# Optimization experiments

Hardware: AMD Instinct MI355X
Metric: run time of the kernel (lower is better)

Reference implementation:

```python
import jax, jax.numpy as jnp
import numpy as np

WEIGHT = 0.1  # init weight

# 6-connectivity (scipy generate_binary_structure(3,1)) neighbor reductions

def _nmin(x, fill):
    p = jnp.pad(x, 1, constant_values=fill)
    return jnp.minimum(
        jnp.minimum(jnp.minimum(p[:-2, 1:-1, 1:-1], p[2:, 1:-1, 1:-1]),
                    jnp.minimum(p[1:-1, :-2, 1:-1], p[1:-1, 2:, 1:-1])),
        jnp.minimum(p[1:-1, 1:-1, :-2], p[1:-1, 1:-1, 2:]))


def _nor(x):
    p = jnp.pad(x, 1, constant_values=False)
    return (p[:-2, 1:-1, 1:-1] | p[2:, 1:-1, 1:-1] |
            p[1:-1, :-2, 1:-1] | p[1:-1, 2:, 1:-1] |
            p[1:-1, 1:-1, :-2] | p[1:-1, 1:-1, 2:])


def _nand(x):
    # border_value=0 in scipy.binary_erosion -> pad with False
    p = jnp.pad(x, 1, constant_values=False)
    return (p[:-2, 1:-1, 1:-1] & p[2:, 1:-1, 1:-1] &
            p[1:-1, :-2, 1:-1] & p[1:-1, 2:, 1:-1] &
            p[1:-1, 1:-1, :-2] & p[1:-1, 1:-1, 2:])


def _cc_count(mask):
    # connected-component count via min-label propagation (6-connectivity),
    # equivalent to scipy.ndimage.label(...)[1]
    n = mask.size
    idx = jnp.arange(n, dtype=jnp.int32).reshape(mask.shape)
    big = jnp.int32(n)
    lbl0 = jnp.where(mask, idx, big)

    def body(c):
        lbl, _ = c
        new = jnp.where(mask, jnp.minimum(lbl, _nmin(lbl, big)), big)
        return new, jnp.any(new != lbl)

    lbl, _ = jax.lax.while_loop(lambda c: c[1], body, (lbl0, jnp.bool_(True)))
    # roots: voxels whose label equals their own index
    return jnp.sum(mask & (lbl == idx)).astype(jnp.int32)


def _cavity_volume(mask):
    # binary_fill_holes: background not reachable from the border
    bg = ~mask
    border = jnp.ones(mask.shape, bool).at[1:-1, 1:-1, 1:-1].set(False)
    r0 = bg & border

    def body(c):
        r, _ = c
        new = bg & (r | _nor(r))
        return new, jnp.any(new != r)

    reach, _ = jax.lax.while_loop(lambda c: c[1], body, (r0, jnp.bool_(True)))
    return jnp.sum(bg & ~reach).astype(jnp.int32)


def _betti(mask):
    b0 = _cc_count(mask)
    eroded = mask & _nand(mask)  # binary_erosion, iterations=1
    b0e = _cc_count(eroded)
    b1 = jnp.maximum(jnp.int32(0), b0 - b0e)
    b2 = _cavity_volume(mask) // 100
    return jnp.stack([b0, b1, b2]).astype(jnp.float32)


def setup_inputs() -> dict:
    key = jax.random.key(0)
    k1, k2 = jax.random.split(key)
    B, C, D, H, W = 2, 4, 64, 128, 128
    pred = jax.random.normal(k1, (B, C, D, H, W), dtype=jnp.float32)
    target = jax.random.randint(k2, (B, D, H, W), 0, C, dtype=jnp.int32)
    return {"pred": pred, "target": target}


def reference(pred, target):
    B, C = pred.shape[0], pred.shape[1]
    vol = pred.shape[2:]
    prob = jax.nn.softmax(pred, axis=1)
    # foreground classes 1..C-1, flattened to [B*(C-1), D, H, W]
    pred_masks = (prob[:, 1:] > 0.5).reshape((-1,) + vol)
    cls = jnp.arange(1, C, dtype=target.dtype).reshape(1, C - 1, 1, 1, 1)
    tgt_masks = (target[:, None] == cls).reshape((-1,) + vol)
    pb = jax.vmap(_betti)(pred_masks)  # [B*(C-1), 3]
    tb = jax.vmap(_betti)(tgt_masks)
    count = B * (C - 1)
    return WEIGHT * jnp.abs(pb - tb).sum() / count
```

## Files before the change

### kernel.cpp

```cpp
#include <hip/hip_runtime.h>
#include <stdint.h>

#define DD 64
#define HH 128
#define WW 128
#define NVOX (DD * HH * WW)
#define NWRD (NVOX / 32)
#define BATCH 2
#define NCLS 4
#define NMASK 12
#define NPROB 36
#define NTILE 128
#define MAXC 2048
#define VNODE (NTILE * MAXC)
#define NODE_STRIDE (VNODE + 64)
#define NTASKW 7424

__device__ __forceinline__ int uf_find(int* P, int x) {
    while (true) {
        int p = P[x];
        if (p == x) return x;
        int gp = P[p];
        if (gp != p) P[x] = gp;
        x = gp;
    }
}
__device__ __forceinline__ int uf_find_ro(const int* P, int x) {
    int p;
    while ((p = P[x]) != x) x = p;
    return x;
}
__device__ __forceinline__ void uf_union(int* P, int a, int b) {
    while (true) {
        a = uf_find(P, a);
        b = uf_find(P, b);
        if (a == b) return;
        int lo = a < b ? a : b;
        int hi = a < b ? b : a;
        int old = atomicCAS(&P[hi], hi, lo);
        if (old == hi) return;
        a = lo; b = old;
    }
}

#define SW(v) ((v) + ((v) >> 5))
__device__ __forceinline__ int lfind(int* lp, int x) {
    while (true) {
        int p = lp[SW(x)];
        if (p == x) return x;
        int gp = lp[SW(p)];
        if (gp != p) lp[SW(x)] = gp;
        x = gp;
    }
}
__device__ __forceinline__ void lunion(int* lp, int a, int b) {
    while (true) {
        a = lfind(lp, a);
        b = lfind(lp, b);
        if (a == b) return;
        int lo = a < b ? a : b;
        int hi = a < b ? b : a;
        int old = atomicCAS(&lp[SW(hi)], hi, lo);
        if (old == hi) return;
        a = lo; b = old;
    }
}
__device__ __forceinline__ int lresolve(const int* lp, int h) {
    int v = lp[SW(h)];
    while (v >= 0) v = lp[SW(v)];
    return -v - 1;
}
__device__ __forceinline__ int run_head(uint32_t w, int p) {
    uint32_t below = ~w & ((1u << p) - 1u);
    return below ? (32 - __clz((int)below)) : 0;
}

__device__ __forceinline__ uint32_t ld_word(const uint32_t* __restrict__ maskW,
                                            const uint32_t* __restrict__ erodW,
                                            int phase, int m, int w) {
    if (phase == 0) return maskW[m * NWRD + w];
    if (phase == 1) return erodW[m * NWRD + w];
    return ~maskW[m * NWRD + w];
}


__global__ void k_masks2(const float* __restrict__ pred, const int* __restrict__ tgt,
                         uint32_t* __restrict__ maskW, int* __restrict__ counts) {
    int tid = blockIdx.x * blockDim.x + threadIdx.x;
    if (tid < 64) counts[tid] = 0;
    int b = tid >> 20;
    int i = tid & (NVOX - 1);
    const float* p = pred + (size_t)b * NCLS * NVOX + i;
    float x0 = p[0], x1 = p[NVOX], x2 = p[2 * NVOX], x3 = p[3 * NVOX];
    float mx = fmaxf(fmaxf(x0, x1), fmaxf(x2, x3));
    float e0 = __expf(x0 - mx), e1 = __expf(x1 - mx), e2 = __expf(x2 - mx), e3 = __expf(x3 - mx);
    float S = e0 + e1 + e2 + e3;
    int t = tgt[(size_t)b * NVOX + i];
    int lane = threadIdx.x & 63;
    int wbase = i >> 5;
    float ev[3] = {e1, e2, e3};
    for (int c = 0; c < 3; ++c) {
        unsigned long long bal = __ballot(ev[c] / S > 0.5f);
        uint32_t* M = maskW + (size_t)(b * 3 + c) * NWRD;
        if (lane == 0)  M[wbase] = (uint32_t)bal;
        if (lane == 32) M[wbase] = (uint32_t)(bal >> 32);
        unsigned long long balT = __ballot(t == c + 1);
        uint32_t* MT = maskW + (size_t)(6 + b * 3 + c) * NWRD;
        if (lane == 0)  MT[wbase] = (uint32_t)balT;
        if (lane == 32) MT[wbase] = (uint32_t)(balT >> 32);
    }
}

__global__ void k_erode(const uint32_t* __restrict__ maskW, uint32_t* __restrict__ erodW) {
    int tid = blockIdx.x * blockDim.x + threadIdx.x;
    int m = tid / NWRD;
    int w = tid - m * NWRD;
    const uint32_t* M = maskW + (size_t)m * NWRD;
    int z = w >> 9, y = (w >> 2) & 127, q = w & 3;
    uint32_t a = M[w];
    uint32_t xl = (a << 1) | (q ? (M[w - 1] >> 31) : 0u);
    uint32_t xr = (a >> 1) | (q < 3 ? (M[w + 1] << 31) : 0u);
    uint32_t ym = (y > 0)   ? M[w - 4]   : 0u;
    uint32_t yp = (y < 127) ? M[w + 4]   : 0u;
    uint32_t zm = (z > 0)   ? M[w - 512] : 0u;
    uint32_t zp = (z < 63)  ? M[w + 512] : 0u;
    erodW[tid] = a & xl & xr & ym & yp & zm & zp;
}

__global__ void k_local(const uint32_t* __restrict__ maskW, const uint32_t* __restrict__ erodW,
                        uint16_t* __restrict__ C16all, int* __restrict__ Pall,
                        uint16_t* __restrict__ volAll, int* __restrict__ tcount, int m0) {
    __shared__ int lp[8448];
    __shared__ uint32_t aw[256];
    __shared__ uint32_t lvol[MAXC / 2];
    __shared__ int lcount;
    int slot = blockIdx.y;
    int pr = m0 + slot;
    int phase = pr / 12, m = pr % 12;
    uint16_t* C16 = C16all + (size_t)slot * NVOX;
    int* P = Pall + (size_t)slot * NODE_STRIDE;
    int tile = blockIdx.x;
    int tz = tile >> 4, ty = tile & 15;
    int t2 = threadIdx.x;
    int lane = t2 & 63;
    int wl = t2 >> 1;
    int h  = t2 & 1;
    int zl = wl >> 5, yl = (wl >> 2) & 7, q = wl & 3;
    int gw = ((tz * 8 + zl) * 128 + (ty * 8 + yl)) * 4 + q;
    uint32_t afull = ld_word(maskW, erodW, phase, m, gw);
    if (h == 0) aw[wl] = afull;
    uint32_t a16 = (afull >> (16 * h)) & 0xFFFFu;
    if (t2 == 0) lcount = 0;
    if (tile == 0 && t2 == 0) P[VNODE] = VNODE;

    int lbase = t2 << 4;
    uint32_t heads = a16 & ~(a16 << 1) & 0xFFFFu;
    {
        uint32_t st = heads;
        while (st) { int p = __ffs(st) - 1; st &= st - 1; lp[SW(lbase + p)] = lbase + p; }
    }
    __syncthreads();

    if (a16) {
        if (a16 & 1u) {
            if (h == 1) {
                uint32_t lo16 = afull & 0xFFFFu;
                if (lo16 >> 15) lunion(lp, lbase, lbase - 16 + run_head(lo16, 15));
            } else if (q) {
                uint32_t hi16 = aw[wl - 1] >> 16;
                if (hi16 >> 15) lunion(lp, lbase, lbase - 16 + run_head(hi16, 15));
            }
        }
        if (yl < 7) {
            uint32_t by = (aw[wl + 4] >> (16 * h)) & 0xFFFFu;
            uint32_t ov = a16 & by;
            uint32_t st = ov & ~(ov << 1);
            int la = -1, lb = -1;
            while (st) {
                int p = __ffs(st) - 1; st &= st - 1;
                int ha = lbase + run_head(a16, p);
                int hb = lbase + 128 + run_head(by, p);
                if (ha != la || hb != lb) { lunion(lp, ha, hb); la = ha; lb = hb; }
            }
        }
        if (zl < 7) {
            uint32_t bz = (aw[wl + 32] >> (16 * h)) & 0xFFFFu;
            uint32_t ov = a16 & bz;
            uint32_t st = ov & ~(ov << 1);
            int la = -1, lb = -1;
            while (st) {
                int p = __ffs(st) - 1; st &= st - 1;
                int ha = lbase + run_head(a16, p);
                int hb = lbase + 1024 + run_head(bz, p);
                if (ha != la || hb != lb) { lunion(lp, ha, hb); la = ha; lb = hb; }
            }
        }
    }
    __syncthreads();

    if (phase == 2) { lvol[t2] = 0; lvol[t2 + 512] = 0; }

    int tileBase = tile * MAXC;
    {
        uint32_t rootMask = 0; int nr = 0;
        uint32_t st = heads;
        while (st) {
            int p = __ffs(st) - 1; st &= st - 1;
            int hh = lbase + p;
            if (lp[SW(hh)] == hh) { rootMask |= 1u << p; ++nr; }
        }
        int pre = nr;
        for (int off = 1; off < 64; off <<= 1) {
            int v = __shfl_up(pre, off);
            if (lane >= off) pre += v;
        }
        int waveTot = __shfl(pre, 63);
        int base = 0;
        if (lane == 63 && waveTot) base = atomicAdd(&lcount, waveTot);
        base = __shfl(base, 63);
        int k = base + pre - nr;
        st = rootMask;
        while (st) {
            int p = __ffs(st) - 1; st &= st - 1;
            int hh = lbase + p;
            lp[SW(hh)] = -k - 1;
            P[tileBase + k] = tileBase + k;
            ++k;
        }
    }
    __syncthreads();

    if (t2 == 0) tcount[slot * NTILE + tile] = lcount;

    int myId = -1, myLen = 0; bool multi = false;
    bool faceRow = (yl == 0 || yl == 7 || zl == 0 || zl == 7);
    if (a16 && (phase == 2 || faceRow)) {
        int i0 = (gw << 5) + 16 * h;
        int gz = tz * 8 + zl, gy = ty * 8 + yl;
        bool bordRow = (phase == 2) && (gz == 0 || gz == 63 || gy == 0 || gy == 127);
        if (faceRow && a16 == 0xFFFFu) {
            int id = lresolve(lp, lbase);
            uint32_t pk = (uint32_t)id * 0x10001u;
            uint4 v = make_uint4(pk, pk, pk, pk);
            uint4* dst = (uint4*)(C16 + i0);
            dst[0] = v; dst[1] = v;
            if (phase == 2) {
                myId = id; myLen = 16;
                if (bordRow || (q == 0 && h == 0) || (q == 3 && h == 1))
                    P[tileBase + id] = VNODE;
            }
        } else {
            int htop = (a16 >> 15) ? run_head(a16, 15) : -1;
            uint32_t st = heads;
            while (st) {
                int p = __ffs(st) - 1; st &= st - 1;
                int id = lresolve(lp, lbase + p);
                uint32_t run = a16 >> p;
                int len = __ffs(~run) - 1;
                if (faceRow) {
                    C16[i0 + p] = (uint16_t)id;
                    for (int j = 1; j < len; ++j) C16[i0 + p + j] = (uint16_t)id;
                }
                if (phase == 2) {
                    if (myLen == 0) myId = id;
                    else if (id != myId) multi = true;
                    myLen += len;
                    if (bordRow || (q == 0 && h == 0 && p == 0) ||
                        (q == 3 && h == 1 && p == htop))
                        P[tileBase + id] = VNODE;
                }
            }
        }
    }

    if (phase == 2) {
        unsigned long long hasMask = __ballot(myLen > 0);
        if (hasMask) {
            bool anyMulti = __any(multi);
            int firstLane = __ffsll(hasMask) - 1;
            int leadId = __shfl(myId, firstLane);
            bool uni = !anyMulti && __all(myLen == 0 || myId == leadId);
            if (uni) {
                int s = myLen;
                for (int off = 32; off; off >>= 1) s += __shfl_down(s, off);
                if (lane == 0 && s)
                    atomicAdd(&lvol[leadId >> 1], (uint32_t)s << ((leadId & 1) * 16));
            } else if (myLen > 0) {
                if (!multi) {
                    atomicAdd(&lvol[myId >> 1], (uint32_t)myLen << ((myId & 1) * 16));
                } else {
                    uint32_t st = heads;
                    while (st) {
                        int p = __ffs(st) - 1; st &= st - 1;
                        int id = lresolve(lp, lbase + p);
                        uint32_t run = a16 >> p;
                        int len = __ffs(~run) - 1;
                        atomicAdd(&lvol[id >> 1], (uint32_t)len << ((id & 1) * 16));
                    }
                }
            }
        }
    }
    __syncthreads();

    if (phase == 2) {
        uint16_t* volC = volAll + (size_t)slot * (NTILE * MAXC) + tileBase;
        for (int k = t2; k < lcount; k += 512)
            volC[k] = (uint16_t)((lvol[k >> 1] >> ((k & 1) * 16)) & 0xFFFFu);
    }
}

__global__ void k_bmerge(const uint32_t* __restrict__ maskW, const uint32_t* __restrict__ erodW,
                         const uint16_t* __restrict__ C16all, int* __restrict__ Pall,
                         int m0) {
    int t = blockIdx.x * blockDim.x + threadIdx.x;
    int slot = blockIdx.y;
    int pr = m0 + slot;
    int phase = pr / 12, m = pr % 12;
    bool act = (t < NTASKW);

    int w = 0, dw = 4, dv = WW, tA = 0, tB = 0;
    if (act) {
        if (t < 3840) {
            int q = t & 3, r = t >> 2;
            int yi = r >> 6, z = r & 63;
            int y = 8 * yi + 7;
            w = (z * 128 + y) * 4 + q;
            dw = 4; dv = WW;
            tA = ((z >> 3) * 16 + yi) * MAXC;
            tB = tA + MAXC;
        } else {
            int tt = t - 3840;
            int q = tt & 3, r = tt >> 2;
            int zi = r >> 7, y = r & 127;
            int z = 8 * zi + 7;
            w = (z * 128 + y) * 4 + q;
            dw = 512; dv = HH * WW;
            tA = (zi * 16 + (y >> 3)) * MAXC;
            tB = tA + 16 * MAXC;
        }
    }

    uint32_t ov = 0;
    if (act) {
        uint32_t a = ld_word(maskW, erodW, phase, m, w);
        if (a) {
            uint32_t b = ld_word(maskW, erodW, phase, m, w + dw);
            ov = a & b;
        }
    }

    const uint16_t* C16 = C16all + (size_t)slot * NVOX;
    int* P = Pall + (size_t)slot * NODE_STRIDE;
    int i0 = w << 5;
    uint32_t st = ov & ~(ov << 1);

    int ca = -1, cb = -1, p0 = -1;
    if (st) {
        p0 = __ffs(st) - 1;
        ca = tA + C16[i0 + p0];
        cb = tB + C16[i0 + p0 + dv];
    }
    int la = __shfl_up(ca, 1);
    int lb = __shfl_up(cb, 1);
    if ((threadIdx.x & 63) == 0) { la = -1; lb = -1; }

    while (st) {
        int p = __ffs(st) - 1; st &= st - 1;
        int xa, xb;
        if (p == p0) { xa = ca; xb = cb; }
        else { xa = tA + C16[i0 + p]; xb = tB + C16[i0 + p + dv]; }
        if (xa != la || xb != lb) { uf_union(P, xa, xb); la = xa; lb = xb; }
    }
}

__global__ void k_flatc(const int* __restrict__ Pall, const uint16_t* __restrict__ volAll,
                        const int* __restrict__ tcount, int* __restrict__ counts, int m0) {
    __shared__ int sAcc;
    __shared__ int sRootV;
    int slot = blockIdx.y;
    int pr = m0 + slot;
    int phase = pr / 12;
    int tile = blockIdx.x;
    const int* P = Pall + (size_t)slot * NODE_STRIDE;
    int lc = tcount[slot * NTILE + tile];
    if (threadIdx.x == 0) {
        sAcc = 0;
        sRootV = (phase == 2) ? uf_find_ro(P, VNODE) : 0;
    }
    __syncthreads();
    int cnt = 0;
    if (phase == 2) {
        const uint16_t* volC = volAll + (size_t)slot * (NTILE * MAXC) + tile * MAXC;
        int rootV = sRootV;
        for (int k = threadIdx.x; k < lc; k += blockDim.x) {
            int id = tile * MAXC + k;
            if (uf_find_ro(P, id) != rootV) cnt += volC[k];
        }
    } else {
        for (int k = threadIdx.x; k < lc; k += blockDim.x) {
            int id = tile * MAXC + k;
            if (uf_find_ro(P, id) == id) ++cnt;
        }
    }
    for (int off = 32; off; off >>= 1) cnt += __shfl_down(cnt, off);
    if ((threadIdx.x & 63) == 0 && cnt) atomicAdd(&sAcc, cnt);
    __syncthreads();
    if (threadIdx.x == 0 && sAcc) atomicAdd(&counts[pr], sAcc);
}

__global__ void k_loss(const int* __restrict__ counts, float* __restrict__ out) {
    if (threadIdx.x != 0 || blockIdx.x != 0) return;
    float acc = 0.f;
    for (int m = 0; m < 6; ++m) {
        int pb0 = counts[m],      pbe = counts[12 + m],      pcv = counts[24 + m];
        int tb0 = counts[6 + m],  tbe = counts[12 + 6 + m],  tcv = counts[24 + 6 + m];
        int pb1 = max(0, pb0 - pbe), tb1 = max(0, tb0 - tbe);
        int pb2 = pcv / 100, tb2 = tcv / 100;
        acc += fabsf((float)(pb0 - tb0)) + fabsf((float)(pb1 - tb1)) + fabsf((float)(pb2 - tb2));
    }
    out[0] = 0.1f * acc / 6.0f;
}

extern "C" void kernel_launch(void* const* d_in, const int* in_sizes, int n_in,
                              void* d_out, int out_size, void* d_ws, size_t ws_size,
                              hipStream_t stream) {
    const float* pred = (const float*)d_in[0];
    const int* tgt = (const int*)d_in[1];
    float* out = (float*)d_out;

    uint8_t* ws = (uint8_t*)d_ws;
    uint32_t* maskW = (uint32_t*)ws;
    size_t off = (size_t)NMASK * NWRD * 4;
    uint32_t* erodW = (uint32_t*)(ws + off);
    off += (size_t)NMASK * NWRD * 4;
    int* counts = (int*)(ws + off);
    off += 256;
    int* tcount = (int*)(ws + off);
    off += (size_t)NPROB * NTILE * 4;
    off = (off + 255) & ~(size_t)255;

    size_t avail = ws_size > off ? ws_size - off : 0;
    size_t slot_bytes = (size_t)NVOX * 2 + (size_t)NODE_STRIDE * 4
                      + (size_t)NTILE * MAXC * 2;
    int PB = (int)(avail / slot_bytes);
    if (PB > NPROB) PB = NPROB;
    if (PB < 1) PB = 1;

    uint16_t* C16all = (uint16_t*)(ws + off);
    int* Pall = (int*)(ws + off + (size_t)PB * NVOX * 2);
    uint16_t* volAll = (uint16_t*)(ws + off + (size_t)PB * NVOX * 2
                                   + (size_t)PB * NODE_STRIDE * 4);

    k_masks2<<<dim3((BATCH * NVOX) / 256), 256, 0, stream>>>(pred, tgt, maskW, counts);
    k_erode<<<dim3((NMASK * NWRD) / 256), 256, 0, stream>>>(maskW, erodW);

    for (int m0 = 0; m0 < NPROB; m0 += PB) {
        int mb = PB < (NPROB - m0) ? PB : (NPROB - m0);
        k_local <<<dim3(NTILE, mb), 512, 0, stream>>>(maskW, erodW, C16all, Pall,
                                                      volAll, tcount, m0);
        k_bmerge<<<dim3((NTASKW + 255) / 256, mb), 256, 0, stream>>>(maskW, erodW, C16all,
                                                                     Pall, m0);
        k_flatc <<<dim3(NTILE, mb), 256, 0, stream>>>(Pall, volAll, tcount, counts, m0);
    }

    k_loss<<<1, 64, 0, stream>>>(counts, out);
}
```

Measured before the change: 217.9 us.

## Fuse mask and complement labeling into one combined union-find pass

Labels the foreground components and the background (cavity) components of each mask in a single combined connected-components pass. Foreground IDs grow up from the bottom of each tile's range and background IDs grow down from the top, so one slot now covers both problems and the problem count drops from 36 to 24. It also adds an early exit for empty tiles of eroded masks. In exchange, the combined blocks do more union work per thread and pack two counters into one 32-bit value, which caps each at 16 bits.

```diff
diff --git a/kernel.cpp b/kernel.cpp
--- a/kernel.cpp
+++ b/kernel.cpp
@@ -9,7 +9,7 @@
 #define BATCH 2
 #define NCLS 4
 #define NMASK 12
-#define NPROB 36
+#define NSLOT 24
 #define NTILE 128
 #define MAXC 2048
 #define VNODE (NTILE * MAXC)
@@ -73,14 +73,6 @@
 __device__ __forceinline__ int run_head(uint32_t w, int p) {
     uint32_t below = ~w & ((1u << p) - 1u);
     return below ? (32 - __clz((int)below)) : 0;
-}
-
-__device__ __forceinline__ uint32_t ld_word(const uint32_t* __restrict__ maskW,
-                                            const uint32_t* __restrict__ erodW,
-                                            int phase, int m, int w) {
-    if (phase == 0) return maskW[m * NWRD + w];
-    if (phase == 1) return erodW[m * NWRD + w];
-    return ~maskW[m * NWRD + w];
 }
 
 
@@ -136,7 +128,8 @@
     __shared__ int lcount;
     int slot = blockIdx.y;
     int pr = m0 + slot;
-    int phase = pr / 12, m = pr % 12;
+    bool comb = pr < 12;
+    int m = comb ? pr : pr - 12;
     uint16_t* C16 = C16all + (size_t)slot * NVOX;
     int* P = Pall + (size_t)slot * NODE_STRIDE;
     int tile = blockIdx.x;
@@ -147,21 +140,92 @@
     int h  = t2 & 1;
     int zl = wl >> 5, yl = (wl >> 2) & 7, q = wl & 3;
     int gw = ((tz * 8 + zl) * 128 + (ty * 8 + yl)) * 4 + q;
-    uint32_t afull = ld_word(maskW, erodW, phase, m, gw);
+    uint32_t afull = comb ? maskW[m * NWRD + gw] : erodW[m * NWRD + gw];
     if (h == 0) aw[wl] = afull;
     uint32_t a16 = (afull >> (16 * h)) & 0xFFFFu;
+    uint32_t av = ~a16 & 0xFFFFu;
     if (t2 == 0) lcount = 0;
-    if (tile == 0 && t2 == 0) P[VNODE] = VNODE;
+    if (comb && tile == 0 && t2 == 0) P[VNODE] = VNODE;
+
+    if (!comb) {
+        int any = __syncthreads_count(a16 != 0);
+        if (any == 0) {
+            if (t2 == 0) tcount[slot * NTILE + tile] = 0;
+            return;
+        }
+    }
 
     int lbase = t2 << 4;
-    uint32_t heads = a16 & ~(a16 << 1) & 0xFFFFu;
+    uint32_t heads = comb ? (((a16 ^ (a16 << 1)) | 1u) & 0xFFFFu)
+                          : (a16 & ~(a16 << 1) & 0xFFFFu);
     {
         uint32_t st = heads;
         while (st) { int p = __ffs(st) - 1; st &= st - 1; lp[SW(lbase + p)] = lbase + p; }
     }
     __syncthreads();
 
-    if (a16) {
+    if (comb) {
+        {
+            int v0 = a16 & 1;
+            if (h == 1) {
+                uint32_t lo = afull & 0xFFFFu;
+                if ((int)((lo >> 15) & 1) == v0) {
+                    uint32_t pm = v0 ? lo : (~lo & 0xFFFFu);
+                    lunion(lp, lbase, lbase - 16 + run_head(pm, 15));
+                }
+            } else if (q) {
+                uint32_t hi = aw[wl - 1] >> 16;
+                if ((int)((hi >> 15) & 1) == v0) {
+                    uint32_t pm = v0 ? hi : (~hi & 0xFFFFu);
+                    lunion(lp, lbase, lbase - 16 + run_head(pm, 15));
+                }
+            }
+        }
+        if (yl < 7) {
+            uint32_t nb = (aw[wl + 4] >> (16 * h)) & 0xFFFFu;
+            uint32_t nv = ~nb & 0xFFFFu;
+            uint32_t ov = a16 & nb;
+            uint32_t st = ov & ~(ov << 1);
+            int la = -1, lb = -1;
+            while (st) {
+                int p = __ffs(st) - 1; st &= st - 1;
+                int ha = lbase + run_head(a16, p);
+                int hb = lbase + 128 + run_head(nb, p);
+                if (ha != la || hb != lb) { lunion(lp, ha, hb); la = ha; lb = hb; }
+            }
+            ov = av & nv;
+            st = ov & ~(ov << 1);
+            la = -1; lb = -1;
+            while (st) {
+                int p = __ffs(st) - 1; st &= st - 1;
+                int ha = lbase + run_head(av, p);
+                int hb = lbase + 128 + run_head(nv, p);
+                if (ha != la || hb != lb) { lunion(lp, ha, hb); la = ha; lb = hb; }
+            }
+        }
+        if (zl < 7) {
+            uint32_t nb = (aw[wl + 32] >> (16 * h)) & 0xFFFFu;
+            uint32_t nv = ~nb & 0xFFFFu;
+            uint32_t ov = a16 & nb;
+            uint32_t st = ov & ~(ov << 1);
+            int la = -1, lb = -1;
+            while (st) {
+                int p = __ffs(st) - 1; st &= st - 1;
+                int ha = lbase + run_head(a16, p);
+                int hb = lbase + 1024 + run_head(nb, p);
+                if (ha != la || hb != lb) { lunion(lp, ha, hb); la = ha; lb = hb; }
+            }
+            ov = av & nv;
+            st = ov & ~(ov << 1);
+            la = -1; lb = -1;
+            while (st) {
+                int p = __ffs(st) - 1; st &= st - 1;
+                int ha = lbase + run_head(av, p);
+                int hb = lbase + 1024 + run_head(nv, p);
+                if (ha != la || hb != lb) { lunion(lp, ha, hb); la = ha; lb = hb; }
+            }
+        }
+    } else if (a16) {
         if (a16 & 1u) {
             if (h == 1) {
                 uint32_t lo16 = afull & 0xFFFFu;
@@ -198,18 +262,22 @@
     }
     __syncthreads();
 
-    if (phase == 2) { lvol[t2] = 0; lvol[t2 + 512] = 0; }
+    if (comb) { lvol[t2] = 0; lvol[t2 + 512] = 0; }
 
     int tileBase = tile * MAXC;
     {
-        uint32_t rootMask = 0; int nr = 0;
+        uint32_t rootMask = 0; int nrF = 0, nrB = 0;
         uint32_t st = heads;
         while (st) {
             int p = __ffs(st) - 1; st &= st - 1;
             int hh = lbase + p;
-            if (lp[SW(hh)] == hh) { rootMask |= 1u << p; ++nr; }
-        }
-        int pre = nr;
+            if (lp[SW(hh)] == hh) {
+                rootMask |= 1u << p;
+                if (comb && !((a16 >> p) & 1)) ++nrB; else ++nrF;
+            }
+        }
+        int packed = nrF | (nrB << 16);
+        int pre = packed;
         for (int off = 1; off < 64; off <<= 1) {
             int v = __shfl_up(pre, off);
             if (lane >= off) pre += v;
@@ -218,14 +286,18 @@
         int base = 0;
         if (lane == 63 && waveTot) base = atomicAdd(&lcount, waveTot);
         base = __shfl(base, 63);
-        int k = base + pre - nr;
+        int excl = pre - packed;
+        int kF = (base & 0xFFFF) + (excl & 0xFFFF);
+        int kB = ((unsigned)base >> 16) + ((unsigned)excl >> 16);
         st = rootMask;
         while (st) {
             int p = __ffs(st) - 1; st &= st - 1;
             int hh = lbase + p;
-            lp[SW(hh)] = -k - 1;
-            P[tileBase + k] = tileBase + k;
-            ++k;
+            int id;
+            if (!comb || ((a16 >> p) & 1)) id = kF++;
+            else                           id = MAXC - 1 - (kB++);
+            lp[SW(hh)] = -id - 1;
+            P[tileBase + id] = tileBase + id;
         }
     }
     __syncthreads();
@@ -234,46 +306,49 @@
 
     int myId = -1, myLen = 0; bool multi = false;
     bool faceRow = (yl == 0 || yl == 7 || zl == 0 || zl == 7);
-    if (a16 && (phase == 2 || faceRow)) {
+    if (comb || (a16 && faceRow)) {
         int i0 = (gw << 5) + 16 * h;
         int gz = tz * 8 + zl, gy = ty * 8 + yl;
-        bool bordRow = (phase == 2) && (gz == 0 || gz == 63 || gy == 0 || gy == 127);
-        if (faceRow && a16 == 0xFFFFu) {
+        bool bordRow = comb && (gz == 0 || gz == 63 || gy == 0 || gy == 127);
+        bool uniHalf = (a16 == 0xFFFFu) || (comb && a16 == 0);
+        if (faceRow && uniHalf) {
             int id = lresolve(lp, lbase);
             uint32_t pk = (uint32_t)id * 0x10001u;
-            uint4 v = make_uint4(pk, pk, pk, pk);
+            uint4 v4 = make_uint4(pk, pk, pk, pk);
             uint4* dst = (uint4*)(C16 + i0);
-            dst[0] = v; dst[1] = v;
-            if (phase == 2) {
+            dst[0] = v4; dst[1] = v4;
+            if (comb && a16 == 0) {
                 myId = id; myLen = 16;
                 if (bordRow || (q == 0 && h == 0) || (q == 3 && h == 1))
                     P[tileBase + id] = VNODE;
             }
         } else {
-            int htop = (a16 >> 15) ? run_head(a16, 15) : -1;
-            uint32_t st = heads;
-            while (st) {
-                int p = __ffs(st) - 1; st &= st - 1;
+            uint32_t it = comb ? (faceRow ? heads : (heads & av)) : heads;
+            int htopB = (comb && !((a16 >> 15) & 1)) ? run_head(av, 15) : -1;
+            while (it) {
+                int p = __ffs(it) - 1; it &= it - 1;
+                int vbit = comb ? (int)((a16 >> p) & 1) : 1;
+                uint32_t mv = vbit ? a16 : av;
                 int id = lresolve(lp, lbase + p);
-                uint32_t run = a16 >> p;
+                uint32_t run = mv >> p;
                 int len = __ffs(~run) - 1;
                 if (faceRow) {
                     C16[i0 + p] = (uint16_t)id;
                     for (int j = 1; j < len; ++j) C16[i0 + p + j] = (uint16_t)id;
                 }
-                if (phase == 2) {
+                if (comb && !vbit) {
                     if (myLen == 0) myId = id;
                     else if (id != myId) multi = true;
                     myLen += len;
                     if (bordRow || (q == 0 && h == 0 && p == 0) ||
-                        (q == 3 && h == 1 && p == htop))
+                        (q == 3 && h == 1 && p == htopB))
                         P[tileBase + id] = VNODE;
                 }
             }
         }
     }
 
-    if (phase == 2) {
+    if (comb) {
         unsigned long long hasMask = __ballot(myLen > 0);
         if (hasMask) {
             bool anyMulti = __any(multi);
@@ -289,11 +364,11 @@
                 if (!multi) {
                     atomicAdd(&lvol[myId >> 1], (uint32_t)myLen << ((myId & 1) * 16));
                 } else {
-                    uint32_t st = heads;
+                    uint32_t st = heads & av;
                     while (st) {
                         int p = __ffs(st) - 1; st &= st - 1;
                         int id = lresolve(lp, lbase + p);
-                        uint32_t run = a16 >> p;
+                        uint32_t run = av >> p;
                         int len = __ffs(~run) - 1;
                         atomicAdd(&lvol[id >> 1], (uint32_t)len << ((id & 1) * 16));
                     }
@@ -303,10 +378,13 @@
     }
     __syncthreads();
 
-    if (phase == 2) {
+    if (comb) {
+        int lcB = lcount >> 16;
         uint16_t* volC = volAll + (size_t)slot * (NTILE * MAXC) + tileBase;
-        for (int k = t2; k < lcount; k += 512)
-            volC[k] = (uint16_t)((lvol[k >> 1] >> ((k & 1) * 16)) & 0xFFFFu);
+        for (int k = t2; k < lcB; k += 512) {
+            int idx = MAXC - 1 - k;
+            volC[idx] = (uint16_t)((lvol[idx >> 1] >> ((idx & 1) * 16)) & 0xFFFFu);
+        }
     }
 }
 
@@ -316,7 +394,8 @@
     int t = blockIdx.x * blockDim.x + threadIdx.x;
     int slot = blockIdx.y;
     int pr = m0 + slot;
-    int phase = pr / 12, m = pr % 12;
+    bool comb = pr < 12;
+    int m = comb ? pr : pr - 12;
     bool act = (t < NTASKW);
 
     int w = 0, dw = 4, dv = WW, tA = 0, tB = 0;
@@ -341,19 +420,27 @@
         }
     }
 
-    uint32_t ov = 0;
+    uint32_t st = 0;
     if (act) {
-        uint32_t a = ld_word(maskW, erodW, phase, m, w);
-        if (a) {
-            uint32_t b = ld_word(maskW, erodW, phase, m, w + dw);
-            ov = a & b;
+        if (comb) {
+            uint32_t a = maskW[m * NWRD + w];
+            uint32_t b = maskW[m * NWRD + w + dw];
+            uint32_t eq = ~(a ^ b);
+            uint32_t tr = (a ^ (a << 1)) | (b ^ (b << 1)) | 1u;
+            st = eq & tr;
+        } else {
+            uint32_t a = erodW[m * NWRD + w];
+            if (a) {
+                uint32_t b = erodW[m * NWRD + w + dw];
+                uint32_t ov = a & b;
+                st = ov & ~(ov << 1);
+            }
         }
     }
 
     const uint16_t* C16 = C16all + (size_t)slot * NVOX;
     int* P = Pall + (size_t)slot * NODE_STRIDE;
     int i0 = w << 5;
-    uint32_t st = ov & ~(ov << 1);
 
     int ca = -1, cb = -1, p0 = -1;
     if (st) {
@@ -380,33 +467,44 @@
     __shared__ int sRootV;
     int slot = blockIdx.y;
     int pr = m0 + slot;
-    int phase = pr / 12;
+    bool comb = pr < 12;
+    int m = comb ? pr : pr - 12;
     int tile = blockIdx.x;
     const int* P = Pall + (size_t)slot * NODE_STRIDE;
-    int lc = tcount[slot * NTILE + tile];
+    int tc = tcount[slot * NTILE + tile];
+    int lcF = tc & 0xFFFF, lcB = (unsigned)tc >> 16;
     if (threadIdx.x == 0) {
         sAcc = 0;
-        sRootV = (phase == 2) ? uf_find_ro(P, VNODE) : 0;
+        sRootV = comb ? uf_find_ro(P, VNODE) : 0;
     }
     __syncthreads();
+    int tileBase = tile * MAXC;
     int cnt = 0;
-    if (phase == 2) {
-        const uint16_t* volC = volAll + (size_t)slot * (NTILE * MAXC) + tile * MAXC;
+    for (int k = threadIdx.x; k < lcF; k += blockDim.x) {
+        int id = tileBase + k;
+        if (uf_find_ro(P, id) == id) ++cnt;
+    }
+    if (comb && lcB) {
+        const uint16_t* volC = volAll + (size_t)slot * (NTILE * MAXC) + tileBase;
         int rootV = sRootV;
-        for (int k = threadIdx.x; k < lc; k += blockDim.x) {
-            int id = tile * MAXC + k;
-            if (uf_find_ro(P, id) != rootV) cnt += volC[k];
-        }
-    } else {
-        for (int k = threadIdx.x; k < lc; k += blockDim.x) {
-            int id = tile * MAXC + k;
-            if (uf_find_ro(P, id) == id) ++cnt;
+        for (int k = threadIdx.x; k < lcB; k += blockDim.x) {
+            int idx = MAXC - 1 - k;
+            if (uf_find_ro(P, tileBase + idx) != rootV) cnt += (int)volC[idx] << 16;
         }
     }
     for (int off = 32; off; off >>= 1) cnt += __shfl_down(cnt, off);
     if ((threadIdx.x & 63) == 0 && cnt) atomicAdd(&sAcc, cnt);
     __syncthreads();
-    if (threadIdx.x == 0 && sAcc) atomicAdd(&counts[pr], sAcc);
+    if (threadIdx.x == 0 && sAcc) {
+        int f = sAcc & 0xFFFF;
+        int v = (unsigned)sAcc >> 16;
+        if (comb) {
+            if (f) atomicAdd(&counts[m], f);
+            if (v) atomicAdd(&counts[24 + m], v);
+        } else if (f) {
+            atomicAdd(&counts[12 + m], f);
+        }
+    }
 }
 
 __global__ void k_loss(const int* __restrict__ counts, float* __restrict__ out) {
@@ -437,14 +535,14 @@
     int* counts = (int*)(ws + off);
     off += 256;
     int* tcount = (int*)(ws + off);
-    off += (size_t)NPROB * NTILE * 4;
+    off += (size_t)NSLOT * NTILE * 4;
     off = (off + 255) & ~(size_t)255;
 
     size_t avail = ws_size > off ? ws_size - off : 0;
     size_t slot_bytes = (size_t)NVOX * 2 + (size_t)NODE_STRIDE * 4
                       + (size_t)NTILE * MAXC * 2;
     int PB = (int)(avail / slot_bytes);
-    if (PB > NPROB) PB = NPROB;
+    if (PB > NSLOT) PB = NSLOT;
     if (PB < 1) PB = 1;
 
     uint16_t* C16all = (uint16_t*)(ws + off);
@@ -455,8 +553,8 @@
     k_masks2<<<dim3((BATCH * NVOX) / 256), 256, 0, stream>>>(pred, tgt, maskW, counts);
     k_erode<<<dim3((NMASK * NWRD) / 256), 256, 0, stream>>>(maskW, erodW);
 
-    for (int m0 = 0; m0 < NPROB; m0 += PB) {
-        int mb = PB < (NPROB - m0) ? PB : (NPROB - m0);
+    for (int m0 = 0; m0 < NSLOT; m0 += PB) {
+        int mb = PB < (NSLOT - m0) ? PB : (NSLOT - m0);
         k_local <<<dim3(NTILE, mb), 512, 0, stream>>>(maskW, erodW, C16all, Pall,
                                                       volAll, tcount, m0);
         k_bmerge<<<dim3((NTASKW + 255) / 256, mb), 256, 0, stream>>>(maskW, erodW, C16all,
```

Measured after the change: 243.8 us. 1.12x slower.
